# Kernel tuning notes

Measured on AMD Instinct MI355X. Metric: run time of the kernel, lower is better.

## Reference

```python
import jax, jax.numpy as jnp
import numpy as np

EPS = 1e-5


def setup_inputs() -> dict:
    key = jax.random.key(0)
    ks = jax.random.split(key, 5)
    B, C, H, W = 64, 512, 28, 28
    G = 8
    c_half = C // (2 * G)  # 32
    return {
        "x": jax.random.normal(ks[0], (B, C, H, W), dtype=jnp.float32),
        "cweight": jax.random.normal(ks[1], (c_half,), dtype=jnp.float32),
        "cbias": jax.random.normal(ks[2], (c_half,), dtype=jnp.float32),
        "sweight": jax.random.normal(ks[3], (c_half,), dtype=jnp.float32),
        "sbias": jax.random.normal(ks[4], (c_half,), dtype=jnp.float32),
        "G": G,
    }


def reference(x, cweight, cbias, sweight, sbias, G):
    B, C, H, W = x.shape
    HW = H * W
    Cg = C // G
    c_half = Cg // 2

    # group view: [B*G, Cg, HW]
    xg = x.reshape(B * G, Cg, HW)
    x0 = xg[:, :c_half]   # channel-attention half
    x1 = xg[:, c_half:]   # spatial-attention half

    # channel attention: sigmoid(cweight * avgpool_hw(x0) + cbias), per channel
    m = jnp.mean(x0, axis=-1, keepdims=True)                    # [BG, c_half, 1]
    a0 = jax.nn.sigmoid(cweight[None, :, None] * m + cbias[None, :, None])
    y0 = x0 * a0

    # spatial attention: GN stats over the whole c_half*HW slab per (b,g)
    mu = jnp.mean(x1, axis=(1, 2), keepdims=True)               # [BG, 1, 1]
    var = jnp.mean(x1 * x1, axis=(1, 2), keepdims=True) - mu * mu
    rstd = jax.lax.rsqrt(jnp.maximum(var, 0.0) + EPS)
    norm = (x1 - mu) * rstd
    a1 = jax.nn.sigmoid(sweight[None, :, None] * norm + sbias[None, :, None])
    y1 = x1 * a1

    y = jnp.concatenate([y0, y1], axis=1).reshape(B, C, HW)

    # channel shuffle with 2 groups: out[:, 2*w + g2] = y[:, g2*(C//2) + w]
    y = y.reshape(B, 2, C // 2, HW).transpose(0, 2, 1, 3).reshape(B, C, H, W)
    return y
```

## Files before the change

kernel.cpp:

```cpp
#include <hip/hip_runtime.h>

typedef float f32x4 __attribute__((ext_vector_type(4)));
typedef float f32x2 __attribute__((ext_vector_type(2)));

#define EPSV 1e-5f

__device__ __forceinline__ float sigmoidf_(float z) {
    return 1.0f / (1.0f + __expf(-z));
}

__global__ __launch_bounds__(256) void gate_stats_kernel(
    const f32x4* __restrict__ x4,
    const float* __restrict__ cweight,
    const float* __restrict__ cbias,
    const float* __restrict__ sweight,
    const float* __restrict__ sbias,
    f32x4* __restrict__ out4,
    f32x2* __restrict__ wsAB,
    int nA)
{
    if ((int)blockIdx.x < nA) {
        const int w  = blockIdx.x * 4 + (threadIdx.x >> 6);
        const int ln = threadIdx.x & 63;
        const int bg = w >> 5;
        const int cc = w & 31;

        const f32x4* __restrict__ xch = x4 + (size_t)bg * 12544 + cc * 196;
        f32x4 v0 = xch[ln];
        f32x4 v1 = xch[64 + ln];
        f32x4 v2 = xch[128 + ln];
        f32x4 v3 = {0.f, 0.f, 0.f, 0.f};
        const bool extra = (ln < 4);
        if (extra) v3 = xch[192 + ln];

        float s = (v0.x + v0.y) + (v0.z + v0.w)
                + (v1.x + v1.y) + (v1.z + v1.w)
                + (v2.x + v2.y) + (v2.z + v2.w)
                + (v3.x + v3.y) + (v3.z + v3.w);
#pragma unroll
        for (int m = 32; m >= 1; m >>= 1) s += __shfl_xor(s, m, 64);

        const float a0 = sigmoidf_(cweight[cc] * (s * (1.0f / 784.0f)) + cbias[cc]);

        const int b = bg >> 3, g = bg & 7;
        const int c  = g * 64 + cc;
        const int cp = (c < 256) ? (2 * c) : (2 * (c - 256) + 1);
        f32x4* __restrict__ och = out4 + (size_t)b * 100352 + (size_t)cp * 196;

        __builtin_nontemporal_store(v0 * a0, &och[ln]);
        __builtin_nontemporal_store(v1 * a0, &och[64 + ln]);
        __builtin_nontemporal_store(v2 * a0, &och[128 + ln]);
        if (extra) __builtin_nontemporal_store(v3 * a0, &och[192 + ln]);
    } else {
        const int bg  = (int)blockIdx.x - nA;
        const int tid = threadIdx.x;
        const f32x4* __restrict__ xs = x4 + (size_t)bg * 12544 + 6272;

        float s = 0.f, ss = 0.f;
#pragma unroll
        for (int k = 0; k < 24; ++k) {
            f32x4 v = xs[tid + 256 * k];
            s  += (v.x + v.y) + (v.z + v.w);
            ss += (v.x * v.x + v.y * v.y) + (v.z * v.z + v.w * v.w);
        }
        if (tid < 128) {
            f32x4 v = xs[6144 + tid];
            s  += (v.x + v.y) + (v.z + v.w);
            ss += (v.x * v.x + v.y * v.y) + (v.z * v.z + v.w * v.w);
        }

#pragma unroll
        for (int m = 32; m >= 1; m >>= 1) {
            s  += __shfl_xor(s,  m, 64);
            ss += __shfl_xor(ss, m, 64);
        }

        __shared__ float lds_s[4], lds_ss[4], lds_st[2];
        const int wv = tid >> 6;
        if ((tid & 63) == 0) { lds_s[wv] = s; lds_ss[wv] = ss; }
        __syncthreads();
        if (tid == 0) {
            const float S  = (lds_s[0] + lds_s[1]) + (lds_s[2] + lds_s[3]);
            const float SS = (lds_ss[0] + lds_ss[1]) + (lds_ss[2] + lds_ss[3]);
            constexpr float inv_n = 1.0f / (32.0f * 784.0f);
            const float mu   = S * inv_n;
            const float var  = SS * inv_n - mu * mu;
            const float rstd = rsqrtf(fmaxf(var, 0.f) + EPSV);
            lds_st[0] = mu; lds_st[1] = rstd;
        }
        __syncthreads();
        if (tid < 32) {
            const float mu = lds_st[0], rstd = lds_st[1];
            const float A  = sweight[tid] * rstd;
            f32x2 ab; ab.x = A; ab.y = sbias[tid] - A * mu;
            wsAB[bg * 32 + tid] = ab;
        }
    }
}

__global__ __launch_bounds__(256) void apply1_kernel(
    const f32x4* __restrict__ x4,
    const f32x2* __restrict__ wsAB,
    f32x4* __restrict__ out4,
    int total)
{
    for (int i = blockIdx.x * 256 + threadIdx.x; i < total;
         i += gridDim.x * 256) {
        const int bg  = i / 6272;
        const int rem = i - bg * 6272;
        const int c1  = rem / 196;
        const int p   = rem - c1 * 196;

        const f32x4 v = x4[(size_t)bg * 12544 + 6272 + rem];
        const f32x2 ab = wsAB[bg * 32 + c1];

        f32x4 r;
        r.x = v.x * sigmoidf_(ab.x * v.x + ab.y);
        r.y = v.y * sigmoidf_(ab.x * v.y + ab.y);
        r.z = v.z * sigmoidf_(ab.x * v.z + ab.y);
        r.w = v.w * sigmoidf_(ab.x * v.w + ab.y);

        const int b = bg >> 3, g = bg & 7;
        const int c  = g * 64 + 32 + c1;
        const int cp = (c < 256) ? (2 * c) : (2 * (c - 256) + 1);
        __builtin_nontemporal_store(
            r, out4 + (size_t)b * 100352 + (size_t)cp * 196 + p);
    }
}

extern "C" void kernel_launch(void* const* d_in, const int* in_sizes, int n_in,
                              void* d_out, int out_size, void* d_ws, size_t ws_size,
                              hipStream_t stream) {
    const float* x  = (const float*)d_in[0];
    const float* cw = (const float*)d_in[1];
    const float* cb = (const float*)d_in[2];
    const float* sw = (const float*)d_in[3];
    const float* sb = (const float*)d_in[4];
    float* out = (float*)d_out;

    const int B  = in_sizes[0] / (512 * 784);
    const int nA = B * 64;
    const int nB = B * 8;

    gate_stats_kernel<<<nA + nB, 256, 0, stream>>>(
        (const f32x4*)x, cw, cb, sw, sb,
        (f32x4*)out, (f32x2*)d_ws, nA);

    const int total1 = B * 8 * 6272;
    apply1_kernel<<<2048, 256, 0, stream>>>(
        (const f32x4*)x, (const f32x2*)d_ws, (f32x4*)out, total1);
}
```

Measured before the change: 199.9 us.

## Fuse spatial-gate stats and apply into one register-resident pass

Merges the stats kernel and the separate apply kernel so each 1024-thread block loads its group's spatial half once into registers, computes GroupNorm stats via block reduction, then applies the gate and writes the shuffled output. The channel-attention half is handled by other blocks of the same launch, now 16 channels per block. This removes the second global read of the spatial half, the workspace round-trip and one kernel launch. It adds register pressure and a block-wide barrier stall while the whole slab is held live.

```diff
diff --git a/kernel.cpp b/kernel.cpp
--- a/kernel.cpp
+++ b/kernel.cpp
@@ -1,7 +1,6 @@
 #include <hip/hip_runtime.h>
 
 typedef float f32x4 __attribute__((ext_vector_type(4)));
-typedef float f32x2 __attribute__((ext_vector_type(2)));
 
 #define EPSV 1e-5f
 
@@ -9,28 +8,111 @@
     return 1.0f / (1.0f + __expf(-z));
 }
 
-__global__ __launch_bounds__(256) void gate_stats_kernel(
+__global__ __launch_bounds__(1024, 4) void fused_sgate_onepass(
     const f32x4* __restrict__ x4,
     const float* __restrict__ cweight,
     const float* __restrict__ cbias,
     const float* __restrict__ sweight,
     const float* __restrict__ sbias,
     f32x4* __restrict__ out4,
-    f32x2* __restrict__ wsAB,
-    int nA)
+    int nX1)
 {
-    if ((int)blockIdx.x < nA) {
-        const int w  = blockIdx.x * 4 + (threadIdx.x >> 6);
-        const int ln = threadIdx.x & 63;
-        const int bg = w >> 5;
-        const int cc = w & 31;
+    const int tid = threadIdx.x;
+
+    if ((int)blockIdx.x < nX1) {
+        const int bg = blockIdx.x;
+        const int b  = bg >> 3, g = bg & 7;
+        const f32x4* __restrict__ xs = x4 + (size_t)bg * 12544 + 6272;
+
+        f32x4 w[6];
+#pragma unroll
+        for (int k = 0; k < 6; ++k) w[k] = xs[tid + 1024 * k];
+        const bool x1e = (tid < 128);
+        f32x4 we = {0.f, 0.f, 0.f, 0.f};
+        if (x1e) we = xs[6144 + tid];
+
+        float s = 0.f, ss = 0.f;
+#pragma unroll
+        for (int k = 0; k < 6; ++k) {
+            s  += (w[k].x + w[k].y) + (w[k].z + w[k].w);
+            ss += (w[k].x * w[k].x + w[k].y * w[k].y)
+                + (w[k].z * w[k].z + w[k].w * w[k].w);
+        }
+        s  += (we.x + we.y) + (we.z + we.w);
+        ss += (we.x * we.x + we.y * we.y) + (we.z * we.z + we.w * we.w);
+
+#pragma unroll
+        for (int m = 32; m >= 1; m >>= 1) {
+            s  += __shfl_xor(s,  m, 64);
+            ss += __shfl_xor(ss, m, 64);
+        }
+
+        __shared__ float lds_s[16], lds_ss[16];
+        __shared__ float ldsA[32], ldsB[32];
+        if ((tid & 63) == 0) { lds_s[tid >> 6] = s; lds_ss[tid >> 6] = ss; }
+        __syncthreads();
+
+        if (tid < 32) {
+            float S = 0.f, SS = 0.f;
+#pragma unroll
+            for (int i = 0; i < 16; ++i) { S += lds_s[i]; SS += lds_ss[i]; }
+            constexpr float inv_n = 1.0f / (32.0f * 784.0f);
+            const float mu   = S * inv_n;
+            const float var  = SS * inv_n - mu * mu;
+            const float rstd = rsqrtf(fmaxf(var, 0.f) + EPSV);
+            const float A    = sweight[tid] * rstd;
+            ldsA[tid] = A;
+            ldsB[tid] = sbias[tid] - A * mu;
+        }
+        __syncthreads();
+
+#pragma unroll
+        for (int k = 0; k < 6; ++k)
+            asm volatile("" : "+v"(w[k].x), "+v"(w[k].y),
+                              "+v"(w[k].z), "+v"(w[k].w));
+
+        f32x4* __restrict__ ob = out4 + (size_t)b * 100352;
+#pragma unroll
+        for (int k = 0; k < 6; ++k) {
+            const int idx = tid + 1024 * k;
+            const int c1  = idx / 196;
+            const int p   = idx - c1 * 196;
+            const float A = ldsA[c1], Bq = ldsB[c1];
+            f32x4 t = w[k], r;
+            r.x = t.x * sigmoidf_(A * t.x + Bq);
+            r.y = t.y * sigmoidf_(A * t.y + Bq);
+            r.z = t.z * sigmoidf_(A * t.z + Bq);
+            r.w = t.w * sigmoidf_(A * t.w + Bq);
+            const int c  = g * 64 + 32 + c1;
+            const int cp = (c < 256) ? (2 * c) : (2 * (c - 256) + 1);
+            __builtin_nontemporal_store(r, ob + (size_t)cp * 196 + p);
+        }
+        if (x1e) {
+            const int idx = 6144 + tid;
+            const int c1  = idx / 196;
+            const int p   = idx - c1 * 196;
+            const float A = ldsA[c1], Bq = ldsB[c1];
+            f32x4 t = we, r;
+            r.x = t.x * sigmoidf_(A * t.x + Bq);
+            r.y = t.y * sigmoidf_(A * t.y + Bq);
+            r.z = t.z * sigmoidf_(A * t.z + Bq);
+            r.w = t.w * sigmoidf_(A * t.w + Bq);
+            const int c  = g * 64 + 32 + c1;
+            const int cp = (c < 256) ? (2 * c) : (2 * (c - 256) + 1);
+            __builtin_nontemporal_store(r, ob + (size_t)cp * 196 + p);
+        }
+    } else {
+        const int chw = ((int)blockIdx.x - nX1) * 16 + (tid >> 6);
+        const int ln  = tid & 63;
+        const int bg  = chw >> 5;
+        const int cc  = chw & 31;
 
         const f32x4* __restrict__ xch = x4 + (size_t)bg * 12544 + cc * 196;
         f32x4 v0 = xch[ln];
         f32x4 v1 = xch[64 + ln];
         f32x4 v2 = xch[128 + ln];
+        const bool extra = (ln < 4);
         f32x4 v3 = {0.f, 0.f, 0.f, 0.f};
-        const bool extra = (ln < 4);
         if (extra) v3 = xch[192 + ln];
 
         float s = (v0.x + v0.y) + (v0.z + v0.w)
@@ -51,80 +133,6 @@
         __builtin_nontemporal_store(v1 * a0, &och[64 + ln]);
         __builtin_nontemporal_store(v2 * a0, &och[128 + ln]);
         if (extra) __builtin_nontemporal_store(v3 * a0, &och[192 + ln]);
-    } else {
-        const int bg  = (int)blockIdx.x - nA;
-        const int tid = threadIdx.x;
-        const f32x4* __restrict__ xs = x4 + (size_t)bg * 12544 + 6272;
-
-        float s = 0.f, ss = 0.f;
-#pragma unroll
-        for (int k = 0; k < 24; ++k) {
-            f32x4 v = xs[tid + 256 * k];
-            s  += (v.x + v.y) + (v.z + v.w);
-            ss += (v.x * v.x + v.y * v.y) + (v.z * v.z + v.w * v.w);
-        }
-        if (tid < 128) {
-            f32x4 v = xs[6144 + tid];
-            s  += (v.x + v.y) + (v.z + v.w);
-            ss += (v.x * v.x + v.y * v.y) + (v.z * v.z + v.w * v.w);
-        }
-
-#pragma unroll
-        for (int m = 32; m >= 1; m >>= 1) {
-            s  += __shfl_xor(s,  m, 64);
-            ss += __shfl_xor(ss, m, 64);
-        }
-
-        __shared__ float lds_s[4], lds_ss[4], lds_st[2];
-        const int wv = tid >> 6;
-        if ((tid & 63) == 0) { lds_s[wv] = s; lds_ss[wv] = ss; }
-        __syncthreads();
-        if (tid == 0) {
-            const float S  = (lds_s[0] + lds_s[1]) + (lds_s[2] + lds_s[3]);
-            const float SS = (lds_ss[0] + lds_ss[1]) + (lds_ss[2] + lds_ss[3]);
-            constexpr float inv_n = 1.0f / (32.0f * 784.0f);
-            const float mu   = S * inv_n;
-            const float var  = SS * inv_n - mu * mu;
-            const float rstd = rsqrtf(fmaxf(var, 0.f) + EPSV);
-            lds_st[0] = mu; lds_st[1] = rstd;
-        }
-        __syncthreads();
-        if (tid < 32) {
-            const float mu = lds_st[0], rstd = lds_st[1];
-            const float A  = sweight[tid] * rstd;
-            f32x2 ab; ab.x = A; ab.y = sbias[tid] - A * mu;
-            wsAB[bg * 32 + tid] = ab;
-        }
-    }
-}
-
-__global__ __launch_bounds__(256) void apply1_kernel(
-    const f32x4* __restrict__ x4,
-    const f32x2* __restrict__ wsAB,
-    f32x4* __restrict__ out4,
-    int total)
-{
-    for (int i = blockIdx.x * 256 + threadIdx.x; i < total;
-         i += gridDim.x * 256) {
-        const int bg  = i / 6272;
-        const int rem = i - bg * 6272;
-        const int c1  = rem / 196;
-        const int p   = rem - c1 * 196;
-
-        const f32x4 v = x4[(size_t)bg * 12544 + 6272 + rem];
-        const f32x2 ab = wsAB[bg * 32 + c1];
-
-        f32x4 r;
-        r.x = v.x * sigmoidf_(ab.x * v.x + ab.y);
-        r.y = v.y * sigmoidf_(ab.x * v.y + ab.y);
-        r.z = v.z * sigmoidf_(ab.x * v.z + ab.y);
-        r.w = v.w * sigmoidf_(ab.x * v.w + ab.y);
-
-        const int b = bg >> 3, g = bg & 7;
-        const int c  = g * 64 + 32 + c1;
-        const int cp = (c < 256) ? (2 * c) : (2 * (c - 256) + 1);
-        __builtin_nontemporal_store(
-            r, out4 + (size_t)b * 100352 + (size_t)cp * 196 + p);
     }
 }
 
@@ -138,15 +146,10 @@
     const float* sb = (const float*)d_in[4];
     float* out = (float*)d_out;
 
-    const int B  = in_sizes[0] / (512 * 784);
-    const int nA = B * 64;
-    const int nB = B * 8;
+    const int B   = in_sizes[0] / (512 * 784);
+    const int nX1 = B * 8;
+    const int nX0 = B * 16;
 
-    gate_stats_kernel<<<nA + nB, 256, 0, stream>>>(
-        (const f32x4*)x, cw, cb, sw, sb,
-        (f32x4*)out, (f32x2*)d_ws, nA);
-
-    const int total1 = B * 8 * 6272;
-    apply1_kernel<<<2048, 256, 0, stream>>>(
-        (const f32x4*)x, (const f32x2*)d_ws, (f32x4*)out, total1);
+    fused_sgate_onepass<<<nX1 + nX0, 1024, 0, stream>>>(
+        (const f32x4*)x, cw, cb, sw, sb, (f32x4*)out, nX1);
 }
```

New measurement: 193.9 us. 1.03x faster.
